# Optimization experiments

Hardware: AMD Instinct MI355X
Metric: run time of the kernel (lower is better)

The kernel has to match this reference:

```python
import jax, jax.numpy as jnp
import numpy as np
from jax import lax
from jax.scipy.special import logsumexp

# weights from options.loss
W_CHAMFER = 1.0
W_CHAMFER_OPP = 1.0
W_EMD = 1.0
# EMD (entropic OT / Sinkhorn) approximation hyper-params
EMD_EPS = 0.05
EMD_ITERS = 20

B, N, D = 16, 2048, 3


def setup_inputs() -> dict:
    key = jax.random.key(0)
    k1, k2, k3, k4 = jax.random.split(key, 4)
    return {
        "gt_points": jax.random.normal(k1, (B, N, D), dtype=jnp.float32),
        "gt_normals": jax.random.normal(k2, (B, N, D), dtype=jnp.float32),
        "pred_points0": jax.random.normal(k3, (B, N, D), dtype=jnp.float32),
        "pred_points1": jax.random.normal(k4, (B, N, D), dtype=jnp.float32),
        "epoch": 10,
    }


def pairwise_sqdist(x, y):
    # x: [B,N,3], y: [B,M,3] -> [B,N,M] squared euclidean distances
    x2 = jnp.sum(x * x, axis=-1)[:, :, None]
    y2 = jnp.sum(y * y, axis=-1)[:, None, :]
    d = x2 + y2 - 2.0 * jnp.einsum('bnd,bmd->bnm', x, y)
    return jnp.maximum(d, 0.0)


def chamfer_loss(pc1, pc2):
    # ChamferDist: dist1[i] = min_j ||pc1_i - pc2_j||^2, dist2 symmetric
    d = pairwise_sqdist(pc1, pc2)  # [B,N,M]
    dist1 = jnp.min(d, axis=2)
    dist2 = jnp.min(d, axis=1)
    return jnp.mean(dist1) + W_CHAMFER_OPP * jnp.mean(dist2)


def emd_loss(pc1, pc2):
    # Entropic-regularized OT (log-domain Sinkhorn) approximation of EMD
    C = jnp.sqrt(pairwise_sqdist(pc1, pc2) + 1e-12)  # [B,N,M] L2 cost
    b, n, m = C.shape
    log_mu = -jnp.log(jnp.float32(n))  # uniform marginals
    log_nu = -jnp.log(jnp.float32(m))

    def step(carry, _):
        f, g = carry  # dual potentials [B,N], [B,M]
        f = EMD_EPS * log_mu - EMD_EPS * logsumexp((g[:, None, :] - C) / EMD_EPS, axis=2)
        g = EMD_EPS * log_nu - EMD_EPS * logsumexp((f[:, :, None] - C) / EMD_EPS, axis=1)
        return (f, g), None

    init = (jnp.zeros((b, n), C.dtype), jnp.zeros((b, m), C.dtype))
    (f, g), _ = lax.scan(jax.checkpoint(step), init, None, length=EMD_ITERS)
    # transport plan and per-batch transport cost
    P = jnp.exp((f[:, :, None] + g[:, None, :] - C) / EMD_EPS)  # [B,N,M]
    cost = jnp.sum(P * C, axis=(1, 2))  # [B]
    return jnp.mean(cost)


def reference(gt_points, gt_normals, pred_points0, pred_points1, epoch):
    preds = [pred_points0, pred_points1]
    chamfer = 0.0
    emd = 0.0
    for p in preds:
        chamfer = chamfer + chamfer_loss(gt_points, p)
        emd = emd + emd_loss(p, gt_points)
    # uniform_loss and normal_loss stay 0.0 in the original forward
    loss = W_CHAMFER * chamfer + W_EMD * emd
    return loss
```

## Files before the change

### kernel.cpp

```cpp
#include <hip/hip_runtime.h>

#define BATCH 16
#define NPTS  2048
#define NMAT  32
#define ITERS 20

typedef short bf16x8 __attribute__((ext_vector_type(8)));
typedef float f32x4 __attribute__((ext_vector_type(4)));
typedef unsigned short ushort_t;
typedef unsigned int uint_t;

constexpr float KSCALE = 28.853900817779268f;

__device__ __forceinline__ float fexp2(float x){ return __builtin_amdgcn_exp2f(x); }
__device__ __forceinline__ float flog2(float x){ return __builtin_amdgcn_logf(x); }
__device__ __forceinline__ float fsqrt_(float x){ return __builtin_amdgcn_sqrtf(x); }

__device__ __forceinline__ ushort_t bfr16(float x){
  uint_t u = __float_as_uint(x);
  return (ushort_t)((u + 0x7FFFu + ((u >> 16) & 1u)) >> 16);
}
__device__ __forceinline__ float bfrf(float x){
  return __uint_as_float(((uint_t)bfr16(x)) << 16);
}

__device__ __forceinline__ void store_enc(ushort_t* base, int pt, const ushort_t* enc){
  ushort_t* p = base + (pt >> 4) * 512 + (pt & 15) * 8;
#pragma unroll
  for (int g = 0; g < 4; ++g){
    *reinterpret_cast<ushort4*>(p + g*128)     = make_ushort4(enc[g*8+0],enc[g*8+1],enc[g*8+2],enc[g*8+3]);
    *reinterpret_cast<ushort4*>(p + g*128 + 4) = make_ushort4(enc[g*8+4],enc[g*8+5],enc[g*8+6],enc[g*8+7]);
  }
}

__global__ void __launch_bounds__(256) pack_kernel(
    const float* __restrict__ gt, const float* __restrict__ p0, const float* __restrict__ p1,
    ushort_t* __restrict__ Lpred, ushort_t* __restrict__ Rpred,
    ushort_t* __restrict__ Lgt,   ushort_t* __restrict__ Rgt,
    float* __restrict__ emd, float* __restrict__ chamf)
{
  const int idx = blockIdx.x * 256 + threadIdx.x;
  const int totalPts = (NMAT + BATCH) * NPTS;
  if (idx < totalPts) {
    const int cl = idx >> 11, pt = idx & (NPTS - 1);
    const float* src; ushort_t *Lb, *Rb;
    if (cl < NMAT) {
      const int b = cl >> 1;
      src = ((cl & 1) ? p1 : p0) + (b * NPTS + pt) * 3;
      Lb = Lpred + cl * 65536; Rb = Rpred + cl * 65536;
    } else {
      const int b = cl - NMAT;
      src = gt + (b * NPTS + pt) * 3;
      Lb = Lgt + b * 65536; Rb = Rgt + b * 65536;
    }
    float L[32], R[32];
#pragma unroll
    for (int k = 27; k < 32; ++k){ L[k] = 0.f; R[k] = 0.f; }
#pragma unroll
    for (int c = 0; c < 3; ++c){
      const float v  = src[c];
      const float ah = bfrf(v), al = bfrf(v - ah);
      const float n2 = v * v;
      const float nh = bfrf(n2); const float r1 = n2 - nh;
      const float nm = bfrf(r1); const float nl = bfrf(r1 - nm);
      const int B0 = c * 9;
      L[B0+0]=nh;  L[B0+1]=nm;  L[B0+2]=nl;
      L[B0+3]=1.f; L[B0+4]=1.f; L[B0+5]=1.f;
      L[B0+6]=-2.f*ah; L[B0+7]=-2.f*ah; L[B0+8]=-2.f*al;
      R[B0+0]=1.f; R[B0+1]=1.f; R[B0+2]=1.f;
      R[B0+3]=nh;  R[B0+4]=nm;  R[B0+5]=nl;
      R[B0+6]=ah;  R[B0+7]=al;  R[B0+8]=ah;
    }
    ushort_t Le[32], Re[32];
#pragma unroll
    for (int k = 0; k < 32; ++k){ Le[k] = bfr16(L[k]); Re[k] = bfr16(R[k]); }
    store_enc(Lb, pt, Le);
    store_enc(Rb, pt, Re);
  } else if (idx == totalPts) {
    emd[0] = 0.f;
  } else if (idx == totalPts + 1) {
    chamf[0] = 0.f;
  }
}

template<int CHAM, int RPOT, int GSIDE, int COST>
__global__ void __launch_bounds__(512, 8) sink_kernel(
    const ushort_t* __restrict__ Lpred, const ushort_t* __restrict__ Rpred,
    const ushort_t* __restrict__ Lgt,   const ushort_t* __restrict__ Rgt,
    float* __restrict__ FT, float* __restrict__ GT,
    float* __restrict__ chamf, float* __restrict__ emd)
{
  const int bx0 = blockIdx.x;
  const int bx  = (bx0 & 7) * (NMAT * 32 / 8) + (bx0 >> 3);
  const int m   = bx >> 5;
  const int rg5 = bx & 31;
  const int b   = m >> 1;
  const int tid = threadIdx.x;
  const int l   = tid & 63;
  const int w   = __builtin_amdgcn_readfirstlane(tid >> 6);
  const int wr  = w & 3;
  const int half= w >> 2;

  const ushort_t* A  = GSIDE ? (Lgt + b*65536)   : (Lpred + m*65536);
  const ushort_t* Bm = GSIDE ? (Rpred + m*65536) : (Rgt + b*65536);
  const float* pinT  = (GSIDE ? FT : GT) + m*NPTS;
  float*       poutT = (GSIDE ? GT : FT) + m*NPTS;

  const int rowbase = rg5 * 64;
  const int myrow16 = rowbase + wr * 16;

  __shared__ float ssum[8][16];
  __shared__ float sdm[8][16];
  __shared__ float sds[4];

  const bf16x8 af = *reinterpret_cast<const bf16x8*>(A + (myrow16 >> 4) * 512 + l * 8);

  float s0=0.f,s1=0.f,s2=0.f,s3=0.f;
  float d0=1e30f,d1=1e30f,d2=1e30f,d3=1e30f;
  float t0=0.f,t1=0.f,t2=0.f,t3=0.f;
  const f32x4 zz = {0.f,0.f,0.f,0.f};
  const ushort_t* Bu = Bm + half * (64*512);
  const int voff = l * 8;
  const float* PTu = pinT + (half*16)*64 + (l & 15)*4;

  auto tilef = [&](const bf16x8& bfr, float pv) {
    f32x4 d4 = __builtin_amdgcn_mfma_f32_16x16x32_bf16(af, bfr, zz, 0, 0, 0);
    const float da=fmaxf(d4[0],1e-12f), db=fmaxf(d4[1],1e-12f);
    const float dc=fmaxf(d4[2],1e-12f), dd=fmaxf(d4[3],1e-12f);
    if (CHAM){ d0=fminf(d0,da); d1=fminf(d1,db); d2=fminf(d2,dc); d3=fminf(d3,dd); }
    const float Ca=fsqrt_(da), Cb=fsqrt_(db), Cc=fsqrt_(dc), Cd=fsqrt_(dd);
    float ea,eb,ec,ed;
    if (RPOT){
      ea=fmaf(-KSCALE,Ca,pv); eb=fmaf(-KSCALE,Cb,pv);
      ec=fmaf(-KSCALE,Cc,pv); ed=fmaf(-KSCALE,Cd,pv);
    } else {
      ea=-KSCALE*Ca; eb=-KSCALE*Cb; ec=-KSCALE*Cc; ed=-KSCALE*Cd;
    }
    const float xa=fexp2(ea), xb=fexp2(eb), xc=fexp2(ec), xd=fexp2(ed);
    s0+=xa; s1+=xb; s2+=xc; s3+=xd;
    if (COST){
      t0=fmaf(xa,Ca,t0); t1=fmaf(xb,Cb,t1);
      t2=fmaf(xc,Cc,t2); t3=fmaf(xd,Cd,t3);
    }
  };

#pragma unroll 2
  for (int g4 = 0; g4 < 16; ++g4) {
    const ushort_t* Bg = Bu + g4 * (4*512);
    float4 cp;
    if (RPOT) cp = *reinterpret_cast<const float4*>(PTu + g4*64);
    else      cp = make_float4(0.f,0.f,0.f,0.f);
    tilef(*reinterpret_cast<const bf16x8*>(Bg + voff + 0*512), cp.x);
    tilef(*reinterpret_cast<const bf16x8*>(Bg + voff + 1*512), cp.y);
    tilef(*reinterpret_cast<const bf16x8*>(Bg + voff + 2*512), cp.z);
    tilef(*reinterpret_cast<const bf16x8*>(Bg + voff + 3*512), cp.w);
  }

#pragma unroll
  for (int o = 1; o < 16; o <<= 1) {
    s0 += __shfl_xor(s0,o); s1 += __shfl_xor(s1,o);
    s2 += __shfl_xor(s2,o); s3 += __shfl_xor(s3,o);
    if (CHAM){
      d0=fminf(d0,__shfl_xor(d0,o)); d1=fminf(d1,__shfl_xor(d1,o));
      d2=fminf(d2,__shfl_xor(d2,o)); d3=fminf(d3,__shfl_xor(d3,o));
    }
    if (COST){
      t0 += __shfl_xor(t0,o); t1 += __shfl_xor(t1,o);
      t2 += __shfl_xor(t2,o); t3 += __shfl_xor(t3,o);
    }
  }
  if ((l & 15) == 0) {
    const int g = l >> 4;
    ssum[w][g*4+0]=s0; ssum[w][g*4+1]=s1; ssum[w][g*4+2]=s2; ssum[w][g*4+3]=s3;
    if (CHAM){ sdm[w][g*4+0]=d0; sdm[w][g*4+1]=d1; sdm[w][g*4+2]=d2; sdm[w][g*4+3]=d3; }
    if (COST){ sdm[w][g*4+0]=t0; sdm[w][g*4+1]=t1; sdm[w][g*4+2]=t2; sdm[w][g*4+3]=t3; }
  }
  __syncthreads();
  float val = 0.f;
  if (w < 4 && l < 16) {
    const float S = ssum[w][l] + ssum[w+4][l];
    val = -11.0f - flog2(S);
    poutT[rg5*64 + l*4 + w] = val;
  }
  if (CHAM) {
    if (w < 4) {
      float dmr = (l < 16) ? fminf(sdm[w][l], sdm[w+4][l]) : 0.f;
#pragma unroll
      for (int o = 1; o < 16; o <<= 1) dmr += __shfl_xor(dmr, o);
      if (l == 0) sds[w] = dmr;
    }
    __syncthreads();
    if (tid == 0) atomicAdd(chamf, (sds[0]+sds[1])+(sds[2]+sds[3]));
  }
  if (COST) {
    if (w < 4) {
      float cj = (l < 16) ? fexp2(val) * (sdm[w][l] + sdm[w+4][l]) : 0.f;
#pragma unroll
      for (int o = 1; o < 16; o <<= 1) cj += __shfl_xor(cj, o);
      if (l == 0) sds[w] = cj;
    }
    __syncthreads();
    if (tid == 0) atomicAdd(emd, (sds[0]+sds[1])+(sds[2]+sds[3]));
  }
}

__global__ void final_kernel(const float* __restrict__ emd,
                             const float* __restrict__ chamf,
                             float* __restrict__ out)
{
  if (blockIdx.x == 0 && threadIdx.x == 0) {
    out[0] = chamf[0] / (float)(BATCH * NPTS) + emd[0] / (float)BATCH;
  }
}

extern "C" void kernel_launch(void* const* d_in, const int* in_sizes, int n_in,
                              void* d_out, int out_size, void* d_ws, size_t ws_size,
                              hipStream_t stream) {
  (void)in_sizes; (void)n_in; (void)out_size; (void)ws_size;
  const float* gt = (const float*)d_in[0];
  const float* p0 = (const float*)d_in[2];
  const float* p1 = (const float*)d_in[3];

  ushort_t* Lpred = (ushort_t*)d_ws;
  ushort_t* Rpred = Lpred + NMAT * 65536;
  ushort_t* Lgt   = Rpred + NMAT * 65536;
  ushort_t* Rgt   = Lgt + BATCH * 65536;
  float* FT    = (float*)(Rgt + BATCH * 65536);
  float* GT    = FT + NMAT * NPTS;
  float* emd   = GT + NMAT * NPTS;
  float* chamf = emd + 1;

  const int initN = (NMAT + BATCH) * NPTS + 2;
  pack_kernel<<<(initN + 255) / 256, 256, 0, stream>>>(gt, p0, p1, Lpred, Rpred, Lgt, Rgt, emd, chamf);

  const int grid = NMAT * 32;
  sink_kernel<1, 0, 0, 0><<<grid, 512, 0, stream>>>(Lpred, Rpred, Lgt, Rgt, FT, GT, chamf, emd);
  sink_kernel<1, 1, 1, 0><<<grid, 512, 0, stream>>>(Lpred, Rpred, Lgt, Rgt, FT, GT, chamf, emd);
  for (int it = 1; it < ITERS - 1; ++it) {
    sink_kernel<0, 1, 0, 0><<<grid, 512, 0, stream>>>(Lpred, Rpred, Lgt, Rgt, FT, GT, chamf, emd);
    sink_kernel<0, 1, 1, 0><<<grid, 512, 0, stream>>>(Lpred, Rpred, Lgt, Rgt, FT, GT, chamf, emd);
  }
  sink_kernel<0, 1, 0, 0><<<grid, 512, 0, stream>>>(Lpred, Rpred, Lgt, Rgt, FT, GT, chamf, emd);
  sink_kernel<0, 1, 1, 1><<<grid, 512, 0, stream>>>(Lpred, Rpred, Lgt, Rgt, FT, GT, chamf, emd);
  final_kernel<<<1, 64, 0, stream>>>(emd, chamf, (float*)d_out);
}
```

Before: 1.287 ms.

## Fuse Sinkhorn iterations into cooperative persistent kernel with per-matrix barriers

Replaces the 40 separate sink_kernel launches with one cooperative mega_kernel. Blocks loop over all half-iterations and synchronise only the 32 blocks that share a matrix, using an atomic counter barrier in global memory. The aim is to remove per-launch overhead and full-grid drain between phases, since each phase is short. The cost is spin-wait barrier latency and a dependence on all 1024 blocks being co-resident. If the cooperative launch fails, the code falls back to the old multi-launch path.

```diff
diff --git a/kernel.cpp b/kernel.cpp
--- a/kernel.cpp
+++ b/kernel.cpp
@@ -37,7 +37,7 @@
     const float* __restrict__ gt, const float* __restrict__ p0, const float* __restrict__ p1,
     ushort_t* __restrict__ Lpred, ushort_t* __restrict__ Rpred,
     ushort_t* __restrict__ Lgt,   ushort_t* __restrict__ Rgt,
-    float* __restrict__ emd, float* __restrict__ chamf)
+    float* __restrict__ emd, float* __restrict__ chamf, uint_t* __restrict__ mbar)
 {
   const int idx = blockIdx.x * 256 + threadIdx.x;
   const int totalPts = (NMAT + BATCH) * NPTS;
@@ -80,6 +80,153 @@
     emd[0] = 0.f;
   } else if (idx == totalPts + 1) {
     chamf[0] = 0.f;
+  } else if (idx < totalPts + 2 + NMAT) {
+    mbar[idx - totalPts - 2] = 0u;
+  }
+}
+
+template<int CHAM, int COST>
+__device__ __forceinline__ void phase_body(
+    float (&ssum)[8][16], float (&sdm)[8][16], float (&sds)[4],
+    const bf16x8 af, const ushort_t* __restrict__ Bu,
+    const float* __restrict__ PTu, const int rpot,
+    const int l, const int w, const int rg5,
+    float* __restrict__ poutT, float* __restrict__ chamf, float* __restrict__ emd)
+{
+  const int tid = threadIdx.x;
+  float s0=0.f,s1=0.f,s2=0.f,s3=0.f;
+  float d0=1e30f,d1=1e30f,d2=1e30f,d3=1e30f;
+  float t0=0.f,t1=0.f,t2=0.f,t3=0.f;
+  const f32x4 zz = {0.f,0.f,0.f,0.f};
+  const int voff = l * 8;
+
+  auto tilef = [&](const bf16x8& bfr, float pv) {
+    f32x4 d4 = __builtin_amdgcn_mfma_f32_16x16x32_bf16(af, bfr, zz, 0, 0, 0);
+    const float da=fmaxf(d4[0],1e-12f), db=fmaxf(d4[1],1e-12f);
+    const float dc=fmaxf(d4[2],1e-12f), dd=fmaxf(d4[3],1e-12f);
+    if (CHAM){ d0=fminf(d0,da); d1=fminf(d1,db); d2=fminf(d2,dc); d3=fminf(d3,dd); }
+    const float Ca=fsqrt_(da), Cb=fsqrt_(db), Cc=fsqrt_(dc), Cd=fsqrt_(dd);
+    const float xa=fexp2(fmaf(-KSCALE,Ca,pv)), xb=fexp2(fmaf(-KSCALE,Cb,pv));
+    const float xc=fexp2(fmaf(-KSCALE,Cc,pv)), xd=fexp2(fmaf(-KSCALE,Cd,pv));
+    s0+=xa; s1+=xb; s2+=xc; s3+=xd;
+    if (COST){
+      t0=fmaf(xa,Ca,t0); t1=fmaf(xb,Cb,t1);
+      t2=fmaf(xc,Cc,t2); t3=fmaf(xd,Cd,t3);
+    }
+  };
+
+#pragma unroll 2
+  for (int g4 = 0; g4 < 16; ++g4) {
+    const ushort_t* Bg = Bu + g4 * 2048;
+    float4 cp;
+    if (rpot) cp = *reinterpret_cast<const float4*>(PTu + g4*64);
+    else      cp = make_float4(0.f,0.f,0.f,0.f);
+    tilef(*reinterpret_cast<const bf16x8*>(Bg + voff +    0), cp.x);
+    tilef(*reinterpret_cast<const bf16x8*>(Bg + voff +  512), cp.y);
+    tilef(*reinterpret_cast<const bf16x8*>(Bg + voff + 1024), cp.z);
+    tilef(*reinterpret_cast<const bf16x8*>(Bg + voff + 1536), cp.w);
+  }
+
+#pragma unroll
+  for (int o = 1; o < 16; o <<= 1) {
+    s0 += __shfl_xor(s0,o); s1 += __shfl_xor(s1,o);
+    s2 += __shfl_xor(s2,o); s3 += __shfl_xor(s3,o);
+    if (CHAM){
+      d0=fminf(d0,__shfl_xor(d0,o)); d1=fminf(d1,__shfl_xor(d1,o));
+      d2=fminf(d2,__shfl_xor(d2,o)); d3=fminf(d3,__shfl_xor(d3,o));
+    }
+    if (COST){
+      t0 += __shfl_xor(t0,o); t1 += __shfl_xor(t1,o);
+      t2 += __shfl_xor(t2,o); t3 += __shfl_xor(t3,o);
+    }
+  }
+  if ((l & 15) == 0) {
+    const int g = l >> 4;
+    ssum[w][g*4+0]=s0; ssum[w][g*4+1]=s1; ssum[w][g*4+2]=s2; ssum[w][g*4+3]=s3;
+    if (CHAM){ sdm[w][g*4+0]=d0; sdm[w][g*4+1]=d1; sdm[w][g*4+2]=d2; sdm[w][g*4+3]=d3; }
+    if (COST){ sdm[w][g*4+0]=t0; sdm[w][g*4+1]=t1; sdm[w][g*4+2]=t2; sdm[w][g*4+3]=t3; }
+  }
+  __syncthreads();
+  float val = 0.f;
+  if (w < 4 && l < 16) {
+    const float S = ssum[w][l] + ssum[w+4][l];
+    val = -11.0f - flog2(S);
+    poutT[rg5*64 + l*4 + w] = val;
+  }
+  if (CHAM) {
+    if (w < 4) {
+      float dmr = (l < 16) ? fminf(sdm[w][l], sdm[w+4][l]) : 0.f;
+#pragma unroll
+      for (int o = 1; o < 16; o <<= 1) dmr += __shfl_xor(dmr, o);
+      if (l == 0) sds[w] = dmr;
+    }
+    __syncthreads();
+    if (tid == 0) atomicAdd(chamf, (sds[0]+sds[1])+(sds[2]+sds[3]));
+  }
+  if (COST) {
+    if (w < 4) {
+      float cj = (l < 16) ? fexp2(val) * (sdm[w][l] + sdm[w+4][l]) : 0.f;
+#pragma unroll
+      for (int o = 1; o < 16; o <<= 1) cj += __shfl_xor(cj, o);
+      if (l == 0) sds[w] = cj;
+    }
+    __syncthreads();
+    if (tid == 0) atomicAdd(emd, (sds[0]+sds[1])+(sds[2]+sds[3]));
+  }
+}
+
+__global__ void __launch_bounds__(512, 8) mega_kernel(
+    const ushort_t* __restrict__ Lpred, const ushort_t* __restrict__ Rpred,
+    const ushort_t* __restrict__ Lgt,   const ushort_t* __restrict__ Rgt,
+    float* __restrict__ FT, float* __restrict__ GT,
+    float* __restrict__ chamf, float* __restrict__ emd, uint_t* __restrict__ mbar)
+{
+  __shared__ float ssum[8][16], sdm[8][16], sds[4];
+  const int bx0 = blockIdx.x;
+  const int bx  = (bx0 & 7) * (NMAT * 32 / 8) + (bx0 >> 3);
+  const int m = bx >> 5, rg5 = bx & 31, b = m >> 1;
+  const int tid = threadIdx.x, l = tid & 63;
+  const int w = __builtin_amdgcn_readfirstlane(tid >> 6);
+  const int wr = w & 3, half = w >> 2;
+  const int myrow16 = rg5*64 + wr*16;
+
+  const bf16x8 af0 = *reinterpret_cast<const bf16x8*>(Lpred + m*65536 + (myrow16>>4)*512 + l*8);
+  const bf16x8 af1 = *reinterpret_cast<const bf16x8*>(Lgt   + b*65536 + (myrow16>>4)*512 + l*8);
+  const ushort_t* Bu0 = Rgt   + b*65536 + half*32768;
+  const ushort_t* Bu1 = Rpred + m*65536 + half*32768;
+  float* FTm = FT + m*NPTS;
+  float* GTm = GT + m*NPTS;
+  const int ptoff = half*1024 + (l & 15)*4;
+
+  uint_t target = 0;
+  for (int ph = 0; ph < 2*ITERS; ++ph) {
+    const int gside = ph & 1;
+    const bf16x8 af = gside ? af1 : af0;
+    const ushort_t* Bu = gside ? Bu1 : Bu0;
+    const float* PTu = (gside ? FTm : GTm) + ptoff;
+    float* poutT = gside ? GTm : FTm;
+
+    if (ph == 0)
+      phase_body<1,0>(ssum,sdm,sds, af,Bu,PTu,0, l,w,rg5, poutT, chamf, emd);
+    else if (ph == 1)
+      phase_body<1,0>(ssum,sdm,sds, af,Bu,PTu,1, l,w,rg5, poutT, chamf, emd);
+    else if (ph == 2*ITERS-1)
+      phase_body<0,1>(ssum,sdm,sds, af,Bu,PTu,1, l,w,rg5, poutT, chamf, emd);
+    else
+      phase_body<0,0>(ssum,sdm,sds, af,Bu,PTu,1, l,w,rg5, poutT, chamf, emd);
+
+    if (ph < 2*ITERS-1) {
+      __syncthreads();
+      target += 32;
+      if (tid == 0) {
+        __threadfence();
+        __hip_atomic_fetch_add(&mbar[m], 1u, __ATOMIC_RELAXED, __HIP_MEMORY_SCOPE_AGENT);
+        while (__hip_atomic_load(&mbar[m], __ATOMIC_RELAXED, __HIP_MEMORY_SCOPE_AGENT) < target)
+          __builtin_amdgcn_s_sleep(2);
+        __threadfence();
+      }
+      __syncthreads();
+    }
   }
 }
 
@@ -90,118 +237,20 @@
     float* __restrict__ FT, float* __restrict__ GT,
     float* __restrict__ chamf, float* __restrict__ emd)
 {
+  __shared__ float ssum[8][16], sdm[8][16], sds[4];
   const int bx0 = blockIdx.x;
   const int bx  = (bx0 & 7) * (NMAT * 32 / 8) + (bx0 >> 3);
-  const int m   = bx >> 5;
-  const int rg5 = bx & 31;
-  const int b   = m >> 1;
-  const int tid = threadIdx.x;
-  const int l   = tid & 63;
-  const int w   = __builtin_amdgcn_readfirstlane(tid >> 6);
-  const int wr  = w & 3;
-  const int half= w >> 2;
-
-  const ushort_t* A  = GSIDE ? (Lgt + b*65536)   : (Lpred + m*65536);
-  const ushort_t* Bm = GSIDE ? (Rpred + m*65536) : (Rgt + b*65536);
-  const float* pinT  = (GSIDE ? FT : GT) + m*NPTS;
-  float*       poutT = (GSIDE ? GT : FT) + m*NPTS;
-
-  const int rowbase = rg5 * 64;
-  const int myrow16 = rowbase + wr * 16;
-
-  __shared__ float ssum[8][16];
-  __shared__ float sdm[8][16];
-  __shared__ float sds[4];
-
-  const bf16x8 af = *reinterpret_cast<const bf16x8*>(A + (myrow16 >> 4) * 512 + l * 8);
-
-  float s0=0.f,s1=0.f,s2=0.f,s3=0.f;
-  float d0=1e30f,d1=1e30f,d2=1e30f,d3=1e30f;
-  float t0=0.f,t1=0.f,t2=0.f,t3=0.f;
-  const f32x4 zz = {0.f,0.f,0.f,0.f};
-  const ushort_t* Bu = Bm + half * (64*512);
-  const int voff = l * 8;
-  const float* PTu = pinT + (half*16)*64 + (l & 15)*4;
-
-  auto tilef = [&](const bf16x8& bfr, float pv) {
-    f32x4 d4 = __builtin_amdgcn_mfma_f32_16x16x32_bf16(af, bfr, zz, 0, 0, 0);
-    const float da=fmaxf(d4[0],1e-12f), db=fmaxf(d4[1],1e-12f);
-    const float dc=fmaxf(d4[2],1e-12f), dd=fmaxf(d4[3],1e-12f);
-    if (CHAM){ d0=fminf(d0,da); d1=fminf(d1,db); d2=fminf(d2,dc); d3=fminf(d3,dd); }
-    const float Ca=fsqrt_(da), Cb=fsqrt_(db), Cc=fsqrt_(dc), Cd=fsqrt_(dd);
-    float ea,eb,ec,ed;
-    if (RPOT){
-      ea=fmaf(-KSCALE,Ca,pv); eb=fmaf(-KSCALE,Cb,pv);
-      ec=fmaf(-KSCALE,Cc,pv); ed=fmaf(-KSCALE,Cd,pv);
-    } else {
-      ea=-KSCALE*Ca; eb=-KSCALE*Cb; ec=-KSCALE*Cc; ed=-KSCALE*Cd;
-    }
-    const float xa=fexp2(ea), xb=fexp2(eb), xc=fexp2(ec), xd=fexp2(ed);
-    s0+=xa; s1+=xb; s2+=xc; s3+=xd;
-    if (COST){
-      t0=fmaf(xa,Ca,t0); t1=fmaf(xb,Cb,t1);
-      t2=fmaf(xc,Cc,t2); t3=fmaf(xd,Cd,t3);
-    }
-  };
-
-#pragma unroll 2
-  for (int g4 = 0; g4 < 16; ++g4) {
-    const ushort_t* Bg = Bu + g4 * (4*512);
-    float4 cp;
-    if (RPOT) cp = *reinterpret_cast<const float4*>(PTu + g4*64);
-    else      cp = make_float4(0.f,0.f,0.f,0.f);
-    tilef(*reinterpret_cast<const bf16x8*>(Bg + voff + 0*512), cp.x);
-    tilef(*reinterpret_cast<const bf16x8*>(Bg + voff + 1*512), cp.y);
-    tilef(*reinterpret_cast<const bf16x8*>(Bg + voff + 2*512), cp.z);
-    tilef(*reinterpret_cast<const bf16x8*>(Bg + voff + 3*512), cp.w);
-  }
-
-#pragma unroll
-  for (int o = 1; o < 16; o <<= 1) {
-    s0 += __shfl_xor(s0,o); s1 += __shfl_xor(s1,o);
-    s2 += __shfl_xor(s2,o); s3 += __shfl_xor(s3,o);
-    if (CHAM){
-      d0=fminf(d0,__shfl_xor(d0,o)); d1=fminf(d1,__shfl_xor(d1,o));
-      d2=fminf(d2,__shfl_xor(d2,o)); d3=fminf(d3,__shfl_xor(d3,o));
-    }
-    if (COST){
-      t0 += __shfl_xor(t0,o); t1 += __shfl_xor(t1,o);
-      t2 += __shfl_xor(t2,o); t3 += __shfl_xor(t3,o);
-    }
-  }
-  if ((l & 15) == 0) {
-    const int g = l >> 4;
-    ssum[w][g*4+0]=s0; ssum[w][g*4+1]=s1; ssum[w][g*4+2]=s2; ssum[w][g*4+3]=s3;
-    if (CHAM){ sdm[w][g*4+0]=d0; sdm[w][g*4+1]=d1; sdm[w][g*4+2]=d2; sdm[w][g*4+3]=d3; }
-    if (COST){ sdm[w][g*4+0]=t0; sdm[w][g*4+1]=t1; sdm[w][g*4+2]=t2; sdm[w][g*4+3]=t3; }
-  }
-  __syncthreads();
-  float val = 0.f;
-  if (w < 4 && l < 16) {
-    const float S = ssum[w][l] + ssum[w+4][l];
-    val = -11.0f - flog2(S);
-    poutT[rg5*64 + l*4 + w] = val;
-  }
-  if (CHAM) {
-    if (w < 4) {
-      float dmr = (l < 16) ? fminf(sdm[w][l], sdm[w+4][l]) : 0.f;
-#pragma unroll
-      for (int o = 1; o < 16; o <<= 1) dmr += __shfl_xor(dmr, o);
-      if (l == 0) sds[w] = dmr;
-    }
-    __syncthreads();
-    if (tid == 0) atomicAdd(chamf, (sds[0]+sds[1])+(sds[2]+sds[3]));
-  }
-  if (COST) {
-    if (w < 4) {
-      float cj = (l < 16) ? fexp2(val) * (sdm[w][l] + sdm[w+4][l]) : 0.f;
-#pragma unroll
-      for (int o = 1; o < 16; o <<= 1) cj += __shfl_xor(cj, o);
-      if (l == 0) sds[w] = cj;
-    }
-    __syncthreads();
-    if (tid == 0) atomicAdd(emd, (sds[0]+sds[1])+(sds[2]+sds[3]));
-  }
+  const int m = bx >> 5, rg5 = bx & 31, b = m >> 1;
+  const int tid = threadIdx.x, l = tid & 63;
+  const int w = __builtin_amdgcn_readfirstlane(tid >> 6);
+  const int wr = w & 3, half = w >> 2;
+  const int myrow16 = rg5*64 + wr*16;
+  const ushort_t* A  = GSIDE ? (Lgt + b*65536) : (Lpred + m*65536);
+  const ushort_t* Bu = (GSIDE ? (Rpred + m*65536) : (Rgt + b*65536)) + half*32768;
+  const float* PTu = ((GSIDE ? FT : GT) + m*NPTS) + half*1024 + (l&15)*4;
+  float* poutT = (GSIDE ? GT : FT) + m*NPTS;
+  const bf16x8 af = *reinterpret_cast<const bf16x8*>(A + (myrow16>>4)*512 + l*8);
+  phase_body<CHAM,COST>(ssum,sdm,sds, af,Bu,PTu,RPOT, l,w,rg5, poutT, chamf, emd);
 }
 
 __global__ void final_kernel(const float* __restrict__ emd,
@@ -229,18 +278,29 @@
   float* GT    = FT + NMAT * NPTS;
   float* emd   = GT + NMAT * NPTS;
   float* chamf = emd + 1;
-
-  const int initN = (NMAT + BATCH) * NPTS + 2;
-  pack_kernel<<<(initN + 255) / 256, 256, 0, stream>>>(gt, p0, p1, Lpred, Rpred, Lgt, Rgt, emd, chamf);
+  uint_t* mbar = (uint_t*)(chamf + 1);
+
+  const int initN = (NMAT + BATCH) * NPTS + 2 + NMAT;
+  pack_kernel<<<(initN + 255) / 256, 256, 0, stream>>>(
+      gt, p0, p1, Lpred, Rpred, Lgt, Rgt, emd, chamf, mbar);
 
   const int grid = NMAT * 32;
-  sink_kernel<1, 0, 0, 0><<<grid, 512, 0, stream>>>(Lpred, Rpred, Lgt, Rgt, FT, GT, chamf, emd);
-  sink_kernel<1, 1, 1, 0><<<grid, 512, 0, stream>>>(Lpred, Rpred, Lgt, Rgt, FT, GT, chamf, emd);
-  for (int it = 1; it < ITERS - 1; ++it) {
+
+  void* args[] = {(void*)&Lpred, (void*)&Rpred, (void*)&Lgt, (void*)&Rgt,
+                  (void*)&FT, (void*)&GT, (void*)&chamf, (void*)&emd, (void*)&mbar};
+  hipError_t ce = hipLaunchCooperativeKernel(
+      reinterpret_cast<void*>(&mega_kernel), dim3(grid), dim3(512), args, 0, stream);
+  if (ce != hipSuccess) {
+    (void)hipGetLastError();
+    sink_kernel<1, 0, 0, 0><<<grid, 512, 0, stream>>>(Lpred, Rpred, Lgt, Rgt, FT, GT, chamf, emd);
+    sink_kernel<1, 1, 1, 0><<<grid, 512, 0, stream>>>(Lpred, Rpred, Lgt, Rgt, FT, GT, chamf, emd);
+    for (int it = 1; it < ITERS - 1; ++it) {
+      sink_kernel<0, 1, 0, 0><<<grid, 512, 0, stream>>>(Lpred, Rpred, Lgt, Rgt, FT, GT, chamf, emd);
+      sink_kernel<0, 1, 1, 0><<<grid, 512, 0, stream>>>(Lpred, Rpred, Lgt, Rgt, FT, GT, chamf, emd);
+    }
     sink_kernel<0, 1, 0, 0><<<grid, 512, 0, stream>>>(Lpred, Rpred, Lgt, Rgt, FT, GT, chamf, emd);
-    sink_kernel<0, 1, 1, 0><<<grid, 512, 0, stream>>>(Lpred, Rpred, Lgt, Rgt, FT, GT, chamf, emd);
-  }
-  sink_kernel<0, 1, 0, 0><<<grid, 512, 0, stream>>>(Lpred, Rpred, Lgt, Rgt, FT, GT, chamf, emd);
-  sink_kernel<0, 1, 1, 1><<<grid, 512, 0, stream>>>(Lpred, Rpred, Lgt, Rgt, FT, GT, chamf, emd);
+    sink_kernel<0, 1, 1, 1><<<grid, 512, 0, stream>>>(Lpred, Rpred, Lgt, Rgt, FT, GT, chamf, emd);
+  }
+
   final_kernel<<<1, 64, 0, stream>>>(emd, chamf, (float*)d_out);
 }
```

After: 4.065 ms. 3.16x slower.
